# Optimization experiments

Measured on AMD Instinct MI355X. Metric: run time of the kernel, lower is better.

Reference implementation:

```python
import jax, jax.numpy as jnp
import numpy as np

B, S, D, H, E = 4, 2048, 256, 8, 65536
HD = D // H  # head_dim = 32


def _layernorm(x, g, b, eps=1e-5):
    mu = jnp.mean(x, axis=-1, keepdims=True)
    var = jnp.var(x, axis=-1, keepdims=True)
    return (x - mu) * jax.lax.rsqrt(var + eps) * g + b


def setup_inputs() -> dict:
    key = jax.random.key(0)
    ks = jax.random.split(key, 16)
    sd = 1.0 / np.sqrt(D)
    inp = {
        "x": jax.random.normal(ks[0], (B, S, D), jnp.float32),
        "adj_mask": jax.random.uniform(ks[1], (B, S, S)) < 0.05,  # ~32 neighbors/node
        "edge_attr": jax.random.normal(ks[2], (E,), jnp.float32),
        "edge_index": jax.random.randint(ks[3], (2, E), 0, S),
        "ln1_g": jnp.ones((D,), jnp.float32),
        "ln1_b": jnp.zeros((D,), jnp.float32),
        "wq": jax.random.normal(ks[4], (D, D), jnp.float32) * sd,
        "bq": jnp.zeros((D,), jnp.float32),
        "wk": jax.random.normal(ks[5], (D, D), jnp.float32) * sd,
        "bk": jnp.zeros((D,), jnp.float32),
        "wv": jax.random.normal(ks[6], (D, D), jnp.float32) * sd,
        "bv": jnp.zeros((D,), jnp.float32),
        "wo": jax.random.normal(ks[7], (D, D), jnp.float32) * sd,
        "bo": jnp.zeros((D,), jnp.float32),
        "ln2_g": jnp.ones((D,), jnp.float32),
        "ln2_b": jnp.zeros((D,), jnp.float32),
        "w1": jax.random.normal(ks[8], (4 * D, D), jnp.float32) * sd,
        "b1": jnp.zeros((4 * D,), jnp.float32),
        "w2": jax.random.normal(ks[9], (D, 4 * D), jnp.float32) * (1.0 / np.sqrt(4 * D)),
        "b2": jnp.zeros((D,), jnp.float32),
    }
    return inp


def reference(x, adj_mask, edge_attr, edge_index,
              ln1_g, ln1_b, wq, bq, wk, bk, wv, bv, wo, bo,
              ln2_g, ln2_b, w1, b1, w2, b2):
    residual = x
    nx = _layernorm(x, ln1_g, ln1_b)
    # projections (torch Linear: y = x W^T + b)
    q = nx @ wq.T + bq
    k = nx @ wk.T + bk
    v = nx @ wv.T + bv
    # (B,S,D) -> (B,H,S,HD)
    q = q.reshape(B, S, H, HD).transpose(0, 2, 1, 3)
    k = k.reshape(B, S, H, HD).transpose(0, 2, 1, 3)
    v = v.reshape(B, S, H, HD).transpose(0, 2, 1, 3)
    scores = jnp.einsum("bhqd,bhkd->bhqk", q, k) / np.sqrt(HD)
    scores = jnp.where(adj_mask[:, None, :, :], scores, -1e9)
    # edge-attr bias: scatter clipped attr into (S,S), gated per-batch by adj_mask,
    # broadcast over heads (replaces the nested python loop)
    clipped = jnp.clip(edge_attr, -5.0, 5.0)
    bias2d = jnp.zeros((S, S), scores.dtype).at[edge_index[0], edge_index[1]].set(clipped)
    scores = scores + jnp.where(adj_mask, bias2d[None, :, :], 0.0)[:, None, :, :]
    attn = jax.nn.softmax(scores, axis=-1)
    ctx = jnp.einsum("bhqk,bhkd->bhqd", attn, v)
    ctx = ctx.transpose(0, 2, 1, 3).reshape(B, S, D)
    x = residual + (ctx @ wo.T + bo)
    # MLP block (exact GELU, like torch nn.GELU())
    n2 = _layernorm(x, ln2_g, ln2_b)
    h = jax.nn.gelu(n2 @ w1.T + b1, approximate=False)
    x = x + (h @ w2.T + b2)
    return x
```

## Files before the change

kernel.cpp:

```cpp
#include <hip/hip_runtime.h>
#include <stdint.h>

#define S 2048
#define D 256
#define H 8
#define HD 32
#define E_EDGES 65536
#define DFF 1024
#define M_TOK 8192
#define CAPR 192
#define QKVN 768

typedef __attribute__((ext_vector_type(8))) short s16x8;
typedef __attribute__((ext_vector_type(8))) unsigned short u16x8;
typedef __attribute__((ext_vector_type(4))) unsigned short u16x4v;
typedef __attribute__((ext_vector_type(4))) float f32x4;

__device__ __forceinline__ float b2f(unsigned short u){
  union { unsigned int i; float f; } x; x.i = ((unsigned int)u) << 16; return x.f;
}
__device__ __forceinline__ unsigned short f2b(float f){
  union { float f; unsigned int i; } x; x.f = f;
  unsigned int r = x.i + 0x7fffu + ((x.i >> 16) & 1u);
  return (unsigned short)(r >> 16);
}
__device__ __forceinline__ void gload_lds16(const void* g, void* l) {
  __builtin_amdgcn_global_load_lds(
      (const __attribute__((address_space(1))) unsigned int*)g,
      (__attribute__((address_space(3))) unsigned int*)l, 16, 0, 0);
}

__global__ __launch_bounds__(256) void prep_kernel(
    const float* __restrict__ wq, const float* __restrict__ wk,
    const float* __restrict__ wv, const float* __restrict__ wo,
    const float* __restrict__ w1, const float* __restrict__ w2,
    unsigned short* __restrict__ wqkvb, unsigned short* __restrict__ wob,
    unsigned short* __restrict__ w1b, unsigned short* __restrict__ w2b)
{
  const int i = blockIdx.x * 256 + threadIdx.x;
  const float* src; unsigned short* dst; int off;
  if      (i <  16384) { src = wq; dst = wqkvb;            off = i; }
  else if (i <  32768) { src = wk; dst = wqkvb +  65536;   off = i -  16384; }
  else if (i <  49152) { src = wv; dst = wqkvb + 131072;   off = i -  32768; }
  else if (i <  65536) { src = wo; dst = wob;              off = i -  49152; }
  else if (i < 131072) { src = w1; dst = w1b;              off = i -  65536; }
  else                 { src = w2; dst = w2b;              off = i - 131072; }
  const float4 v = ((const float4*)src)[off];
  unsigned short o[4] = { f2b(v.x), f2b(v.y), f2b(v.z), f2b(v.w) };
  *(uint2*)(dst + (size_t)off * 4) = *(const uint2*)o;
}

__global__ __launch_bounds__(192) void bias_kernel(
    const float* __restrict__ bq, const float* __restrict__ bk,
    const float* __restrict__ bv, float* __restrict__ bqkv)
{
  const int i = threadIdx.x;
  if      (i <  64) ((float4*)bqkv)[i] = ((const float4*)bq)[i];
  else if (i < 128) ((float4*)bqkv)[i] = ((const float4*)bk)[i - 64];
  else              ((float4*)bqkv)[i] = ((const float4*)bv)[i - 128];
}

__global__ __launch_bounds__(256) void ln_kernel(
    const float* __restrict__ xf,
    const float* __restrict__ g, const float* __restrict__ bt,
    unsigned short* __restrict__ out)
{
  const int wave = threadIdx.x >> 6;
  const int lane = threadIdx.x & 63;
  const int row = blockIdx.x * 4 + wave;
  const size_t base = (size_t)row * D + lane * 4;
  const float4 u = *(const float4*)(xf + base);
  float v[4] = { u.x, u.y, u.z, u.w };
  float s  = v[0]+v[1]+v[2]+v[3];
  float s2 = v[0]*v[0]+v[1]*v[1]+v[2]*v[2]+v[3]*v[3];
  #pragma unroll
  for (int off=32; off>=1; off>>=1){ s += __shfl_xor(s,off,64); s2 += __shfl_xor(s2,off,64); }
  const float mu  = s * (1.f/D);
  const float var = s2 * (1.f/D) - mu*mu;
  const float rs  = 1.f / sqrtf(var + 1e-5f);
  #pragma unroll
  for (int j=0;j<4;++j){
    const int c = lane*4 + j;
    const float y = (v[j]-mu)*rs*g[c] + bt[c];
    out[(size_t)row*D + c] = f2b(y);
  }
}

template<int BM, int BN, int WR, int WC>
__global__ __launch_bounds__(256) void gemm_lds(
    const unsigned short* __restrict__ A,
    const unsigned short* __restrict__ W,
    const float* __restrict__ bias,
    unsigned short* __restrict__ outb, int obN,
    float* __restrict__ outf,
    float* __restrict__ outkv,
    const float* __restrict__ resf,
    int M, int N, int K, int act)
{
  constexpr int WM = BM / WR, WN = BN / WC;
  constexpr int MI = WM / 16, NI = WN / 16;
  __shared__ unsigned short As[2][BM * 32];
  __shared__ unsigned short Bs[2][BN * 32];
  const int tid  = threadIdx.x;
  const int wave = tid >> 6;
  const int lane = tid & 63;
  const int wr = wave / WC, wc = wave % WC;
  const int m0 = blockIdx.y * BM;
  const int n0 = blockIdx.x * BN;
  const int ldr = lane >> 2;
  const int ldc = (lane & 3) * 8;
  const int fr = lane & 15;
  const int kf = (lane >> 4) * 8;
  f32x4 acc[MI][NI];
  #pragma unroll
  for (int i=0;i<MI;++i)
    #pragma unroll
    for (int j=0;j<NI;++j)
      #pragma unroll
      for (int r=0;r<4;++r) acc[i][j][r] = 0.f;

  auto stage = [&](int buf, int k0) {
    #pragma unroll
    for (int c = wave; c < BM/16; c += 4)
      gload_lds16(A + (size_t)(m0 + c*16 + ldr)*K + k0 + ldc, &As[buf][c*512]);
    #pragma unroll
    for (int c = wave; c < BN/16; c += 4)
      gload_lds16(W + (size_t)(n0 + c*16 + ldr)*K + k0 + ldc, &Bs[buf][c*512]);
  };

  stage(0, 0);
  __syncthreads();
  int cur = 0;
  for (int k0 = 0; k0 < K; k0 += 32) {
    if (k0 + 32 < K) stage(cur ^ 1, k0 + 32);
    s16x8 af[MI], bf[NI];
    #pragma unroll
    for (int i = 0; i < MI; ++i) af[i] = *(const s16x8*)&As[cur][(wr*WM + i*16 + fr)*32 + kf];
    #pragma unroll
    for (int j = 0; j < NI; ++j) bf[j] = *(const s16x8*)&Bs[cur][(wc*WN + j*16 + fr)*32 + kf];
    #pragma unroll
    for (int i = 0; i < MI; ++i)
      #pragma unroll
      for (int j = 0; j < NI; ++j)
        acc[i][j] = __builtin_amdgcn_mfma_f32_16x16x32_bf16(af[i], bf[j], acc[i][j], 0, 0, 0);
    __syncthreads();
    cur ^= 1;
  }
  const int rbase = (lane >> 4) * 4;
  #pragma unroll
  for (int j = 0; j < NI; ++j) {
    const int col = n0 + wc*WN + j*16 + fr;
    const float bvl = bias[col];
    #pragma unroll
    for (int i = 0; i < MI; ++i) {
      #pragma unroll
      for (int r = 0; r < 4; ++r) {
        const int row = m0 + wr*WM + i*16 + rbase + r;
        const size_t off = (size_t)row * N + col;
        float vv = acc[i][j][r] + bvl;
        if (act) vv = 0.5f * vv * (1.0f + erff(vv * 0.70710678118654752f));
        if (resf) vv += resf[off];
        if (outb && col < obN) outb[(size_t)row * obN + col] = f2b(vv);
        if (outf) outf[off] = vv;
        if (outkv && col >= 256) outkv[(size_t)row * 512 + (col - 256)] = vv;
      }
    }
  }
}

__global__ __launch_bounds__(256) void zero_kernel(uint4* __restrict__ p, int n4) {
  int i = blockIdx.x * 256 + threadIdx.x;
  if (i < n4) { uint4 z; z.x=0; z.y=0; z.z=0; z.w=0; p[i] = z; }
}
__global__ __launch_bounds__(256) void scatter_kernel(
    const int* __restrict__ ei, const float* __restrict__ attr,
    unsigned int* __restrict__ packed)
{
  int e = blockIdx.x * 256 + threadIdx.x;
  if (e >= E_EDGES) return;
  int r = ei[e], c = ei[E_EDGES + e];
  float v = attr[e];
  v = fminf(5.f, fmaxf(-5.f, v));
  unsigned int pk = (((unsigned int)e) << 16) | (unsigned int)f2b(v);
  atomicMax(&packed[(size_t)r * S + c], pk);
}

__global__ __launch_bounds__(256) void csr_kernel(
    const int* __restrict__ mask, const unsigned int* __restrict__ packed,
    unsigned int* __restrict__ csr, int* __restrict__ cnts)
{
  __shared__ unsigned short nidx[CAPR];
  __shared__ int wtot[4], wbase[4], cnt_s;
  const int t = threadIdx.x;
  const int wave = t >> 6, lane = t & 63;
  const int bqi = blockIdx.x;
  const int qrow = bqi & (S-1);
  const int* mrow = mask + (size_t)bqi * S;
  const uint4 ma = *(const uint4*)(mrow + t*8);
  const uint4 mb = *(const uint4*)(mrow + t*8 + 4);
  unsigned int mv[8] = { ma.x, ma.y, ma.z, ma.w, mb.x, mb.y, mb.z, mb.w };
  int mycnt = 0;
  #pragma unroll
  for (int j = 0; j < 8; ++j) mycnt += mv[j] ? 1 : 0;
  int inc = mycnt;
  #pragma unroll
  for (int off=1; off<64; off<<=1){ int y = __shfl_up(inc, off, 64); if (lane >= off) inc += y; }
  if (lane == 63) wtot[wave] = inc;
  __syncthreads();
  if (t == 0) { int ss=0; for (int w=0; w<4; ++w){ wbase[w]=ss; ss+=wtot[w]; } cnt_s = ss; }
  __syncthreads();
  int pos = wbase[wave] + inc - mycnt;
  #pragma unroll
  for (int j = 0; j < 8; ++j) {
    if (mv[j]) {
      if (pos < CAPR) nidx[pos] = (unsigned short)(t*8 + j);
      ++pos;
    }
  }
  __syncthreads();
  int cnt = cnt_s; if (cnt > CAPR) cnt = CAPR;
  const int cnt_pad = (cnt + 31) & ~31;
  for (int i = t; i < cnt_pad; i += 256) {
    unsigned int e = 0;
    if (i < cnt) {
      const unsigned int ni = nidx[i];
      e = (ni << 16) | (packed[(size_t)qrow * S + ni] & 0xffffu);
    }
    csr[(size_t)bqi * CAPR + i] = e;
  }
  if (t == 0) cnts[bqi] = cnt;
}

__global__ __launch_bounds__(256) void attn_kernel(
    const unsigned short* __restrict__ qb,
    const float* __restrict__ kvf,
    const unsigned int* __restrict__ csr,
    const int* __restrict__ cnts,
    unsigned short* __restrict__ ctx)
{
  __shared__ unsigned int nle[CAPR];
  __shared__ float sc[CAPR*9];
  __shared__ float red[4*D];
  __shared__ float rsum[H];
  const int t = threadIdx.x;
  const int wave = t >> 6, lane = t & 63;
  const int bqi = blockIdx.x;
  const int b = bqi >> 11;
  const char* kvb = (const char*)(kvf + (size_t)b * S * 512);

  const int cnt = cnts[bqi];
  const int cnt_pad = (cnt + 31) & ~31;
  for (int i = t; i < cnt_pad; i += 256) nle[i] = csr[(size_t)bqi * CAPR + i];

  const int hh = lane >> 3;
  const float scale = 0.17677669529663687f;
  float q4[4];
  {
    const u16x4v qv = *(const u16x4v*)(qb + (size_t)bqi * D + lane * 4);
    #pragma unroll
    for (int j = 0; j < 4; ++j) q4[j] = b2f(qv[j]);
  }
  __syncthreads();

  for (int n0 = wave*8; n0 < cnt_pad; n0 += 32) {
    unsigned int e[8]; float4 kv[8];
    #pragma unroll
    for (int u = 0; u < 8; ++u) e[u] = nle[n0 + u];
    #pragma unroll
    for (int u = 0; u < 8; ++u)
      kv[u] = *(const float4*)(kvb + (size_t)((e[u] >> 16) * 2048u) + lane*16);
    #pragma unroll
    for (int u = 0; u < 8; ++u) {
      float p = q4[0]*kv[u].x + q4[1]*kv[u].y + q4[2]*kv[u].z + q4[3]*kv[u].w;
      p += __shfl_xor(p, 1, 64);
      p += __shfl_xor(p, 2, 64);
      p += __shfl_xor(p, 4, 64);
      if ((lane & 7) == 0) {
        const int n = n0 + u;
        sc[n*9 + hh] = (n < cnt) ? fmaf(p, scale, b2f((unsigned short)(e[u] & 0xffffu))) : 0.f;
      }
    }
  }
  __syncthreads();

  if (cnt > 0) {
    const int h = t >> 5, dd = t & 31;
    float m = -1e30f;
    for (int n = dd; n < cnt; n += 32) m = fmaxf(m, sc[n*9 + h]);
    #pragma unroll
    for (int off=16; off>=1; off>>=1) m = fmaxf(m, __shfl_xor(m, off, 64));
    float sum = 0.f;
    for (int n = dd; n < cnt; n += 32) {
      float ev = __expf(sc[n*9 + h] - m);
      sc[n*9 + h] = ev;
      sum += ev;
    }
    #pragma unroll
    for (int off=16; off>=1; off>>=1) sum += __shfl_xor(sum, off, 64);
    if (dd == 0) rsum[h] = 1.f / sum;
  }
  __syncthreads();

  float a4[4] = {0.f, 0.f, 0.f, 0.f};
  if (cnt > 0) {
    for (int n0 = wave*8; n0 < cnt_pad; n0 += 32) {
      unsigned int e[8]; float4 vv[8];
      #pragma unroll
      for (int u = 0; u < 8; ++u) e[u] = nle[n0 + u];
      #pragma unroll
      for (int u = 0; u < 8; ++u)
        vv[u] = *(const float4*)(kvb + (size_t)((e[u] >> 16) * 2048u) + 1024 + lane*16);
      #pragma unroll
      for (int u = 0; u < 8; ++u) {
        const float p = sc[(n0+u)*9 + hh];
        a4[0] += p * vv[u].x;
        a4[1] += p * vv[u].y;
        a4[2] += p * vv[u].z;
        a4[3] += p * vv[u].w;
      }
    }
  } else {
    for (int n = wave; n < S; n += 4) {
      const float4 vv = *(const float4*)(kvb + (size_t)n * 2048 + 1024 + lane*16);
      a4[0] += vv.x; a4[1] += vv.y; a4[2] += vv.z; a4[3] += vv.w;
    }
    #pragma unroll
    for (int j = 0; j < 4; ++j) a4[j] *= (1.f / S);
    if (t < 8) rsum[t] = 1.f;
  }
  *(f32x4*)&red[wave*D + lane*4] = *(f32x4*)a4;
  __syncthreads();
  const float outv = (red[t] + red[D + t] + red[2*D + t] + red[3*D + t]) * rsum[t >> 5];
  ctx[(size_t)bqi * D + t] = f2b(outv);
}

extern "C" void kernel_launch(void* const* d_in, const int* in_sizes, int n_in,
                              void* d_out, int out_size, void* d_ws, size_t ws_size,
                              hipStream_t stream) {
  const float*          x    = (const float*)d_in[0];
  const int*            mask = (const int*)d_in[1];
  const float*          eat  = (const float*)d_in[2];
  const int*            eidx = (const int*)d_in[3];
  const float*          ln1g = (const float*)d_in[4];
  const float*          ln1b = (const float*)d_in[5];
  const float*          wq   = (const float*)d_in[6];
  const float*          bq   = (const float*)d_in[7];
  const float*          wk   = (const float*)d_in[8];
  const float*          bk   = (const float*)d_in[9];
  const float*          wv   = (const float*)d_in[10];
  const float*          bv   = (const float*)d_in[11];
  const float*          wo   = (const float*)d_in[12];
  const float*          bo   = (const float*)d_in[13];
  const float*          ln2g = (const float*)d_in[14];
  const float*          ln2b = (const float*)d_in[15];
  const float*          w1   = (const float*)d_in[16];
  const float*          b1   = (const float*)d_in[17];
  const float*          w2   = (const float*)d_in[18];
  const float*          b2   = (const float*)d_in[19];
  float* out = (float*)d_out;

  char* ws = (char*)d_ws;
  unsigned short* nx   = (unsigned short*)ws;
  unsigned short* qb   = (unsigned short*)(ws + (4u<<20));
  unsigned short* cx   = (unsigned short*)(ws + (8u<<20));
  float*          x1   = (float*)(ws + (12u<<20));
  unsigned int*   csr  = (unsigned int*)(ws + (12u<<20));
  int*            cnts = (int*)(csr + (size_t)M_TOK * CAPR);
  float*          kvf  = (float*)(ws + (20u<<20));
  unsigned int*   pk   = (unsigned int*)(ws + (20u<<20));
  unsigned short* wqkvb= (unsigned short*)(ws + (36u<<20));
  unsigned short* wob  = wqkvb + (size_t)QKVN*D;
  unsigned short* w1b  = wob + (size_t)D*D;
  unsigned short* w2b  = w1b + (size_t)DFF*D;
  float*          bqkv = (float*)(w2b + (size_t)D*DFF);
  unsigned short* hb   = (unsigned short*)kvf;
  unsigned short* n2   = nx;

  prep_kernel<<<768, 256, 0, stream>>>(wq, wk, wv, wo, w1, w2, wqkvb, wob, w1b, w2b);
  bias_kernel<<<1, 192, 0, stream>>>(bq, bk, bv, bqkv);
  zero_kernel<<<(S*S/4 + 255)/256, 256, 0, stream>>>((uint4*)pk, S*S/4);
  scatter_kernel<<<E_EDGES/256, 256, 0, stream>>>(eidx, eat, pk);
  ln_kernel<<<M_TOK/4, 256, 0, stream>>>(x, ln1g, ln1b, nx);
  csr_kernel<<<M_TOK, 256, 0, stream>>>(mask, pk, csr, cnts);
  gemm_lds<64,128,1,4><<<dim3(QKVN/128, M_TOK/64), 256, 0, stream>>>(
      nx, wqkvb, bqkv, qb, 256, nullptr, kvf, nullptr, M_TOK, QKVN, D, 0);
  attn_kernel<<<M_TOK, 256, 0, stream>>>(qb, kvf, csr, cnts, cx);
  gemm_lds<64,64,2,2><<<dim3(D/64, M_TOK/64), 256, 0, stream>>>(
      cx, wob, bo, nullptr, 0, x1, nullptr, x, M_TOK, D, D, 0);
  ln_kernel<<<M_TOK/4, 256, 0, stream>>>(x1, ln2g, ln2b, n2);
  gemm_lds<128,128,2,2><<<dim3(DFF/128, M_TOK/128), 256, 0, stream>>>(
      n2, w1b, b1, hb, DFF, nullptr, nullptr, nullptr, M_TOK, DFF, D, 1);
  gemm_lds<64,64,2,2><<<dim3(D/64, M_TOK/64), 256, 0, stream>>>(
      hb, w2b, b2, nullptr, 0, out, nullptr, x1, M_TOK, D, DFF, 0);
}
```

Baseline: 194.9 us.

## Fuse attention into single pass with unnormalized exp and bf16 K/V storage

The attention kernel now computes scores, exponentials and the weighted V sum in one pass over neighbours. It drops the separate score buffer, max-reduction and second gather, and normalizes by a per-head sum at the end. K and V are kept in bf16 inside one packed QKV buffer instead of an fp32 KV buffer, which halves gather bytes and removes the extra fp32 write from the QKV GEMM. Skipping max subtraction risks overflow for large scores, and bf16 K/V lowers precision.

```diff
diff --git a/kernel.cpp b/kernel.cpp
--- a/kernel.cpp
+++ b/kernel.cpp
@@ -18,6 +18,12 @@
 
 __device__ __forceinline__ float b2f(unsigned short u){
   union { unsigned int i; float f; } x; x.i = ((unsigned int)u) << 16; return x.f;
+}
+__device__ __forceinline__ float u2f_lo(unsigned int u){
+  union { unsigned int i; float f; } x; x.i = u << 16; return x.f;
+}
+__device__ __forceinline__ float u2f_hi(unsigned int u){
+  union { unsigned int i; float f; } x; x.i = u & 0xffff0000u; return x.f;
 }
 __device__ __forceinline__ unsigned short f2b(float f){
   union { float f; unsigned int i; } x; x.f = f;
@@ -91,9 +97,8 @@
     const unsigned short* __restrict__ A,
     const unsigned short* __restrict__ W,
     const float* __restrict__ bias,
-    unsigned short* __restrict__ outb, int obN,
+    unsigned short* __restrict__ outb,
     float* __restrict__ outf,
-    float* __restrict__ outkv,
     const float* __restrict__ resf,
     int M, int N, int K, int act)
 {
@@ -160,9 +165,8 @@
         float vv = acc[i][j][r] + bvl;
         if (act) vv = 0.5f * vv * (1.0f + erff(vv * 0.70710678118654752f));
         if (resf) vv += resf[off];
-        if (outb && col < obN) outb[(size_t)row * obN + col] = f2b(vv);
+        if (outb) outb[off] = f2b(vv);
         if (outf) outf[off] = vv;
-        if (outkv && col >= 256) outkv[(size_t)row * 512 + (col - 256)] = vv;
       }
     }
   }
@@ -232,105 +236,78 @@
 }
 
 __global__ __launch_bounds__(256) void attn_kernel(
-    const unsigned short* __restrict__ qb,
-    const float* __restrict__ kvf,
+    const unsigned short* __restrict__ qkv,
     const unsigned int* __restrict__ csr,
     const int* __restrict__ cnts,
     unsigned short* __restrict__ ctx)
 {
   __shared__ unsigned int nle[CAPR];
-  __shared__ float sc[CAPR*9];
   __shared__ float red[4*D];
-  __shared__ float rsum[H];
+  __shared__ float wsum[4*64];
   const int t = threadIdx.x;
   const int wave = t >> 6, lane = t & 63;
   const int bqi = blockIdx.x;
   const int b = bqi >> 11;
-  const char* kvb = (const char*)(kvf + (size_t)b * S * 512);
+  const char* base = (const char*)(qkv + (size_t)b * S * QKVN);
 
   const int cnt = cnts[bqi];
   const int cnt_pad = (cnt + 31) & ~31;
   for (int i = t; i < cnt_pad; i += 256) nle[i] = csr[(size_t)bqi * CAPR + i];
 
-  const int hh = lane >> 3;
   const float scale = 0.17677669529663687f;
   float q4[4];
   {
-    const u16x4v qv = *(const u16x4v*)(qb + (size_t)bqi * D + lane * 4);
-    #pragma unroll
-    for (int j = 0; j < 4; ++j) q4[j] = b2f(qv[j]);
-  }
-  __syncthreads();
-
-  for (int n0 = wave*8; n0 < cnt_pad; n0 += 32) {
-    unsigned int e[8]; float4 kv[8];
-    #pragma unroll
-    for (int u = 0; u < 8; ++u) e[u] = nle[n0 + u];
-    #pragma unroll
-    for (int u = 0; u < 8; ++u)
-      kv[u] = *(const float4*)(kvb + (size_t)((e[u] >> 16) * 2048u) + lane*16);
-    #pragma unroll
-    for (int u = 0; u < 8; ++u) {
-      float p = q4[0]*kv[u].x + q4[1]*kv[u].y + q4[2]*kv[u].z + q4[3]*kv[u].w;
-      p += __shfl_xor(p, 1, 64);
-      p += __shfl_xor(p, 2, 64);
-      p += __shfl_xor(p, 4, 64);
-      if ((lane & 7) == 0) {
-        const int n = n0 + u;
-        sc[n*9 + hh] = (n < cnt) ? fmaf(p, scale, b2f((unsigned short)(e[u] & 0xffffu))) : 0.f;
-      }
-    }
-  }
-  __syncthreads();
-
-  if (cnt > 0) {
-    const int h = t >> 5, dd = t & 31;
-    float m = -1e30f;
-    for (int n = dd; n < cnt; n += 32) m = fmaxf(m, sc[n*9 + h]);
-    #pragma unroll
-    for (int off=16; off>=1; off>>=1) m = fmaxf(m, __shfl_xor(m, off, 64));
-    float sum = 0.f;
-    for (int n = dd; n < cnt; n += 32) {
-      float ev = __expf(sc[n*9 + h] - m);
-      sc[n*9 + h] = ev;
-      sum += ev;
-    }
-    #pragma unroll
-    for (int off=16; off>=1; off>>=1) sum += __shfl_xor(sum, off, 64);
-    if (dd == 0) rsum[h] = 1.f / sum;
+    const u16x4v qv = *(const u16x4v*)(qkv + (size_t)bqi * QKVN + lane * 4);
+    #pragma unroll
+    for (int j = 0; j < 4; ++j) q4[j] = b2f(qv[j]) * scale;
   }
   __syncthreads();
 
   float a4[4] = {0.f, 0.f, 0.f, 0.f};
+  float ssum = 0.f;
   if (cnt > 0) {
     for (int n0 = wave*8; n0 < cnt_pad; n0 += 32) {
-      unsigned int e[8]; float4 vv[8];
+      unsigned int e[8]; uint2 kv[8], vv[8];
       #pragma unroll
       for (int u = 0; u < 8; ++u) e[u] = nle[n0 + u];
       #pragma unroll
-      for (int u = 0; u < 8; ++u)
-        vv[u] = *(const float4*)(kvb + (size_t)((e[u] >> 16) * 2048u) + 1024 + lane*16);
-      #pragma unroll
       for (int u = 0; u < 8; ++u) {
-        const float p = sc[(n0+u)*9 + hh];
-        a4[0] += p * vv[u].x;
-        a4[1] += p * vv[u].y;
-        a4[2] += p * vv[u].z;
-        a4[3] += p * vv[u].w;
+        const char* r = base + (size_t)(e[u] >> 16) * 1536u;
+        kv[u] = *(const uint2*)(r +  512 + lane*8);
+        vv[u] = *(const uint2*)(r + 1024 + lane*8);
+      }
+      #pragma unroll
+      for (int u = 0; u < 8; ++u) {
+        float p = q4[0]*u2f_lo(kv[u].x) + q4[1]*u2f_hi(kv[u].x)
+                + q4[2]*u2f_lo(kv[u].y) + q4[3]*u2f_hi(kv[u].y);
+        p += __shfl_xor(p, 1, 64);
+        p += __shfl_xor(p, 2, 64);
+        p += __shfl_xor(p, 4, 64);
+        const float s = p + b2f((unsigned short)(e[u] & 0xffffu));
+        const float ee = (n0 + u < cnt) ? __expf(s) : 0.f;
+        ssum += ee;
+        a4[0] += ee * u2f_lo(vv[u].x);
+        a4[1] += ee * u2f_hi(vv[u].x);
+        a4[2] += ee * u2f_lo(vv[u].y);
+        a4[3] += ee * u2f_hi(vv[u].y);
       }
     }
   } else {
     for (int n = wave; n < S; n += 4) {
-      const float4 vv = *(const float4*)(kvb + (size_t)n * 2048 + 1024 + lane*16);
-      a4[0] += vv.x; a4[1] += vv.y; a4[2] += vv.z; a4[3] += vv.w;
+      const uint2 vv = *(const uint2*)(base + (size_t)n*1536 + 1024 + lane*8);
+      a4[0] += u2f_lo(vv.x); a4[1] += u2f_hi(vv.x);
+      a4[2] += u2f_lo(vv.y); a4[3] += u2f_hi(vv.y);
     }
     #pragma unroll
     for (int j = 0; j < 4; ++j) a4[j] *= (1.f / S);
-    if (t < 8) rsum[t] = 1.f;
+    ssum = 0.25f;
   }
   *(f32x4*)&red[wave*D + lane*4] = *(f32x4*)a4;
-  __syncthreads();
-  const float outv = (red[t] + red[D + t] + red[2*D + t] + red[3*D + t]) * rsum[t >> 5];
+  wsum[wave*64 + lane] = ssum;
+  __syncthreads();
+  const int hs = (t >> 5) * 8;
+  const float denom = wsum[hs] + wsum[64 + hs] + wsum[128 + hs] + wsum[192 + hs];
+  const float outv = (red[t] + red[D + t] + red[2*D + t] + red[3*D + t]) / denom;
   ctx[(size_t)bqi * D + t] = f2b(outv);
 }
 
@@ -361,19 +338,18 @@
 
   char* ws = (char*)d_ws;
   unsigned short* nx   = (unsigned short*)ws;
-  unsigned short* qb   = (unsigned short*)(ws + (4u<<20));
-  unsigned short* cx   = (unsigned short*)(ws + (8u<<20));
-  float*          x1   = (float*)(ws + (12u<<20));
-  unsigned int*   csr  = (unsigned int*)(ws + (12u<<20));
+  unsigned short* qkv  = (unsigned short*)(ws + ( 4u<<20));
+  unsigned short* cx   = (unsigned short*)(ws + (16u<<20));
+  float*          x1   = (float*)(ws + (20u<<20));
+  unsigned int*   csr  = (unsigned int*)(ws + (20u<<20));
   int*            cnts = (int*)(csr + (size_t)M_TOK * CAPR);
-  float*          kvf  = (float*)(ws + (20u<<20));
-  unsigned int*   pk   = (unsigned int*)(ws + (20u<<20));
-  unsigned short* wqkvb= (unsigned short*)(ws + (36u<<20));
+  unsigned int*   pk   = (unsigned int*)(ws + (28u<<20));
+  unsigned short* hb   = (unsigned short*)(ws + (28u<<20));
+  unsigned short* wqkvb= (unsigned short*)(ws + (44u<<20));
   unsigned short* wob  = wqkvb + (size_t)QKVN*D;
   unsigned short* w1b  = wob + (size_t)D*D;
   unsigned short* w2b  = w1b + (size_t)DFF*D;
   float*          bqkv = (float*)(w2b + (size_t)D*DFF);
-  unsigned short* hb   = (unsigned short*)kvf;
   unsigned short* n2   = nx;
 
   prep_kernel<<<768, 256, 0, stream>>>(wq, wk, wv, wo, w1, w2, wqkvb, wob, w1b, w2b);
@@ -383,13 +359,13 @@
   ln_kernel<<<M_TOK/4, 256, 0, stream>>>(x, ln1g, ln1b, nx);
   csr_kernel<<<M_TOK, 256, 0, stream>>>(mask, pk, csr, cnts);
   gemm_lds<64,128,1,4><<<dim3(QKVN/128, M_TOK/64), 256, 0, stream>>>(
-      nx, wqkvb, bqkv, qb, 256, nullptr, kvf, nullptr, M_TOK, QKVN, D, 0);
-  attn_kernel<<<M_TOK, 256, 0, stream>>>(qb, kvf, csr, cnts, cx);
+      nx, wqkvb, bqkv, qkv, nullptr, nullptr, M_TOK, QKVN, D, 0);
+  attn_kernel<<<M_TOK, 256, 0, stream>>>(qkv, csr, cnts, cx);
   gemm_lds<64,64,2,2><<<dim3(D/64, M_TOK/64), 256, 0, stream>>>(
-      cx, wob, bo, nullptr, 0, x1, nullptr, x, M_TOK, D, D, 0);
+      cx, wob, bo, nullptr, x1, x, M_TOK, D, D, 0);
   ln_kernel<<<M_TOK/4, 256, 0, stream>>>(x1, ln2g, ln2b, n2);
   gemm_lds<128,128,2,2><<<dim3(DFF/128, M_TOK/128), 256, 0, stream>>>(
-      n2, w1b, b1, hb, DFF, nullptr, nullptr, nullptr, M_TOK, DFF, D, 1);
+      n2, w1b, b1, hb, nullptr, nullptr, M_TOK, DFF, D, 1);
   gemm_lds<64,64,2,2><<<dim3(D/64, M_TOK/64), 256, 0, stream>>>(
-      hb, w2b, b2, nullptr, 0, out, nullptr, x1, M_TOK, D, DFF, 0);
-}
+      hb, w2b, b2, nullptr, out, x1, M_TOK, D, DFF, 0);
+}
```

After: 173.9 us, median of 2. 1.12x faster.
